# Optimization experiments

Measured on AMD Instinct MI355X. Metric: run time of the kernel, lower is better.

## Reference

```python
import jax, jax.numpy as jnp
import numpy as np

# Grids: sparse_shape=(41,320,320); after spcv1 stride(2,1,1) pad1 k3 -> (21,320,320);
# after spcv2 stride(2,1,1) pad(0,1,1) k3 -> (10,320,320); after spcv3 k(3,1,1) stride(2,1,1) -> (4,320,320)
GRID0 = (41, 320, 320)
GRID1 = (21, 320, 320)
GRID2 = (10, 320, 320)
GRID3 = (4, 320, 320)
T = 3
C_IN = 16
BN_EPS = 1e-3


def _idx_grid(coords, shape):
    g = -np.ones(shape, np.int32)
    g[coords[:, 0], coords[:, 1], coords[:, 2]] = np.arange(len(coords), dtype=np.int32)
    return g


def _subm_nbrs(coords, grid):
    M = len(coords)
    nbr = -np.ones((M, 27), np.int32)
    sh = np.array(grid.shape)
    k = 0
    for dz in (-1, 0, 1):
        for dy in (-1, 0, 1):
            for dx in (-1, 0, 1):
                c = coords + np.array([dz, dy, dx])
                ok = np.all((c >= 0) & (c < sh), axis=1)
                nbr[ok, k] = grid[c[ok, 0], c[ok, 1], c[ok, 2]]
                k += 1
    return nbr


def _spconv_pairs(coords_in, grid_in, out_shape, ksz, stride, pad):
    ksz = np.array(ksz); st = np.array(stride); pd = np.array(pad); osh = np.array(out_shape)
    cands = []
    for kz in range(ksz[0]):
        for ky in range(ksz[1]):
            for kx in range(ksz[2]):
                o = coords_in + pd - np.array([kz, ky, kx])
                ok = np.all(o % st == 0, axis=1)
                o = o[ok] // st
                ok2 = np.all((o >= 0) & (o < osh), axis=1)
                cands.append(o[ok2])
    coords_out = np.unique(np.concatenate(cands, 0), axis=0)
    M = len(coords_out); K = int(np.prod(ksz))
    idx = -np.ones((M, K), np.int32)
    sh = np.array(grid_in.shape)
    k = 0
    for kz in range(ksz[0]):
        for ky in range(ksz[1]):
            for kx in range(ksz[2]):
                ci = coords_out * st - pd + np.array([kz, ky, kx])
                ok = np.all((ci >= 0) & (ci < sh), axis=1)
                idx[ok, k] = grid_in[ci[ok, 0], ci[ok, 1], ci[ok, 2]]
                k += 1
    return coords_out.astype(np.int32), idx


def setup_inputs() -> dict:
    rng = np.random.default_rng(0)
    # clustered lidar-like active voxels
    nC, nP = 60, 150
    centers = np.stack([rng.uniform(6, 35, nC), rng.uniform(12, 308, nC), rng.uniform(12, 308, nC)], 1)
    pts = centers[:, None, :] + rng.normal(size=(nC, nP, 3)) * np.array([1.2, 2.0, 2.0])
    pts = np.clip(np.round(pts).astype(np.int64).reshape(-1, 3), 0, np.array(GRID0) - 1)
    coords0 = np.unique(pts, axis=0)
    g0 = _idx_grid(coords0, GRID0)
    nbr0 = _subm_nbrs(coords0, g0)
    coords1, idx1 = _spconv_pairs(coords0, g0, GRID1, (3, 3, 3), (2, 1, 1), (1, 1, 1))
    g1 = _idx_grid(coords1, GRID1)
    nbr1 = _subm_nbrs(coords1, g1)
    coords2, idx2 = _spconv_pairs(coords1, g1, GRID2, (3, 3, 3), (2, 1, 1), (0, 1, 1))
    g2 = _idx_grid(coords2, GRID2)
    nbr2 = _subm_nbrs(coords2, g2)
    coords3, idx3 = _spconv_pairs(coords2, g2, GRID3, (3, 1, 1), (2, 1, 1), (0, 0, 0))

    def w(K, ci, co):
        return jnp.asarray(rng.standard_normal((K, ci, co)) / np.sqrt(K * ci), jnp.float32)

    def bn(n, c):
        g = rng.uniform(0.5, 1.5, (n, c)); b = rng.standard_normal((n, c)) * 0.1
        m = rng.standard_normal((n, c)) * 0.1; v = rng.uniform(0.5, 1.5, (n, c))
        return jnp.asarray(np.stack([g, b, m, v], 1), jnp.float32)  # [n,4,c]

    return dict(
        voxel_features=jnp.asarray(rng.standard_normal((T, len(coords0), C_IN)), jnp.float32),
        w_subm1=w(27, 16, 32), w_subm2=w(27, 32, 32), w_spcv1=w(27, 32, 64),
        w_subm3=w(27, 64, 64), w_subm4=w(27, 64, 64), w_subm5=w(27, 64, 64),
        w_spcv2=w(27, 64, 64), w_subm6=w(27, 64, 64), w_subm7=w(27, 64, 64), w_subm8=w(27, 64, 64),
        w_spcv3=w(3, 64, 64),
        w_ad1=jnp.asarray(rng.standard_normal((64, 64)) / 8.0, jnp.float32),
        w_ad2=jnp.asarray(rng.standard_normal((64, 64)) / 8.0, jnp.float32),
        bn32=bn(2, 32), bn64=bn(9, 64), bn_ad=bn(1, 64)[0],
        nbr0=jnp.asarray(nbr0), idx1=jnp.asarray(idx1), nbr1=jnp.asarray(nbr1),
        idx2=jnp.asarray(idx2), nbr2=jnp.asarray(nbr2), idx3=jnp.asarray(idx3),
        coords3=jnp.asarray(coords3))


def _bn_eval(x, p):
    g, b, m, v = p
    return (x - m) * (g * jax.lax.rsqrt(v + BN_EPS)) + b


def _gconv(f, idx, w):
    # gather-GEMM: idx [M,K] (-1 = missing), f [Min,Ci], w [K,Ci,Co]
    g = jnp.where((idx >= 0)[:, :, None], f[jnp.clip(idx, 0)], 0.0)  # [M,K,Ci]
    return jnp.einsum('mki,kio->mo', g, w)


def reference(voxel_features, w_subm1, w_subm2, w_spcv1, w_subm3, w_subm4, w_subm5,
              w_spcv2, w_subm6, w_subm7, w_subm8, w_spcv3, w_ad1, w_ad2,
              bn32, bn64, bn_ad, nbr0, idx1, nbr1, idx2, nbr2, idx3, coords3):
    relu = jax.nn.relu
    s0 = s1 = s2 = None  # cached previous-frame sparse features per level
    outs = []
    for t in range(voxel_features.shape[0]):
        a0 = 0.0 if s0 is None else jnp.mean(s0, 0)
        a1 = 0.0 if s1 is None else jnp.mean(s1, 0)
        a2 = 0.0 if s2 is None else jnp.mean(s2, 0)
        x = relu(_bn_eval(_gconv(voxel_features[t], nbr0, w_subm1), bn32[0]))
        x = relu(_bn_eval(_gconv(x, nbr0, w_subm2), bn32[1]))
        x3 = relu(_bn_eval(_gconv(x, idx1, w_spcv1) + a0, bn64[0])); s0 = x3
        x = relu(_bn_eval(_gconv(x3, nbr1, w_subm3), bn64[1]))
        x = relu(_bn_eval(_gconv(x, nbr1, w_subm4), bn64[2]))
        x6 = relu(_bn_eval(_gconv(x, nbr1, w_subm5), bn64[3]))
        x7 = relu(_bn_eval(_gconv(x6, idx2, w_spcv2) + a1, bn64[4])); s1 = x7
        x = relu(_bn_eval(_gconv(x7, nbr2, w_subm6), bn64[5]))
        x = relu(_bn_eval(_gconv(x, nbr2, w_subm7), bn64[6]))
        x10 = relu(_bn_eval(_gconv(x, nbr2, w_subm8), bn64[7]))
        x11 = relu(_bn_eval(_gconv(x10, idx3, w_spcv3) + a2, bn64[8])); s2 = x11
        dense = jnp.zeros(GRID3 + (64,), x11.dtype).at[coords3[:, 0], coords3[:, 1], coords3[:, 2]].set(x11)
        outs.append(dense.transpose(3, 0, 1, 2).reshape(1, 64 * GRID3[0], GRID3[1], GRID3[2]))
        adapt = lambda s: (relu(_bn_eval(s @ w_ad1, bn_ad)) @ w_ad2) / 10.0
        s0, s1, s2 = adapt(s0), adapt(s1), adapt(s2)
    return jnp.stack(outs)
```

## Files before the change

### kernel.cpp

```cpp
#include <hip/hip_runtime.h>


typedef _Float16 f16;
typedef _Float16 f16x8 __attribute__((ext_vector_type(8)));
typedef _Float16 f16x4 __attribute__((ext_vector_type(4)));
typedef float    f32x4 __attribute__((ext_vector_type(4)));

#define BN_EPS_F 1e-3f

__global__ __launch_bounds__(256)
void fill_zero(float4* __restrict__ p, long n4)
{
    long i  = blockIdx.x * 256L + threadIdx.x;
    long st = gridDim.x * 256L;
    float4 z = make_float4(0.f, 0.f, 0.f, 0.f);
    for (; i < n4; i += st) p[i] = z;
}

__global__ __launch_bounds__(256)
void wxform(const float* __restrict__ w, f16* __restrict__ wT, int K, int Ci, int Co)
{
    int i = blockIdx.x * 256 + threadIdx.x;
    int total = K * Ci * Co;
    if (i >= total) return;
    int k  = i / (Ci * Co);
    int r  = i - k * (Ci * Co);
    int ci = r / Co;
    int co = r - ci * Co;
    wT[((size_t)k * Co + co) * Ci + ci] = (f16)w[i];
}

template<int Ci, int Co, int K>
__global__ __launch_bounds__(512)
void gconv_mfma(const f16* __restrict__ fin, const int* __restrict__ idx,
                const f16* __restrict__ wT,
                const float* __restrict__ bnp,
                const float* __restrict__ avec,
                f16* __restrict__ fout, int M)
{
    constexpr int CiP = Ci + 8;
    constexpr int cpr = Ci / 8;
    constexpr int NF  = Co / 16;
    constexpr int KK  = Ci / 32;
    constexpr int KH  = (K + 1) / 2;

    __shared__ f16 Ab[2][64 * CiP];
    __shared__ f16 Bb[2][Co * CiP];

    const int tid  = threadIdx.x;
    const int lane = tid & 63;
    const int wv   = tid >> 6;
    const int g    = wv >> 2;
    const int wq   = wv & 3;
    const int gtid = tid & 255;
    const int m0   = blockIdx.x * 64;
    const int l15  = lane & 15;
    const int kg   = lane >> 4;

    f32x4 acc[NF];
    #pragma unroll
    for (int nf = 0; nf < NF; ++nf) acc[nf] = (f32x4){0.f, 0.f, 0.f, 0.f};

    for (int it = 0; it < KH; ++it) {
        const int  k   = (g == 0) ? it : (KH + it);
        const bool act = (g == 0) || (k < K);
        __syncthreads();
        if (act) {
            for (int i = gtid; i < 64 * cpr; i += 256) {
                int r = i / cpr, q = i - r * cpr;
                int m = m0 + r;
                int n = (m < M) ? idx[(size_t)m * K + k] : -1;
                uint4 v = make_uint4(0u, 0u, 0u, 0u);
                if (n >= 0) v = *(const uint4*)&fin[(size_t)n * Ci + q * 8];
                *(uint4*)&Ab[g][r * CiP + q * 8] = v;
            }
            for (int i = gtid; i < Co * cpr; i += 256) {
                int co = i / cpr, q = i - co * cpr;
                *(uint4*)&Bb[g][co * CiP + q * 8] =
                    *(const uint4*)&wT[((size_t)k * Co + co) * Ci + q * 8];
            }
        }
        __syncthreads();
        if (act) {
            #pragma unroll
            for (int kk = 0; kk < KK; ++kk) {
                f16x8 af = *(const f16x8*)&Ab[g][(wq * 16 + l15) * CiP + kk * 32 + kg * 8];
                #pragma unroll
                for (int nf = 0; nf < NF; ++nf) {
                    f16x8 bf = *(const f16x8*)&Bb[g][(nf * 16 + l15) * CiP + kk * 32 + kg * 8];
                    acc[nf] = __builtin_amdgcn_mfma_f32_16x16x32_f16(af, bf, acc[nf], 0, 0, 0);
                }
            }
        }
    }

    float* red = (float*)&Ab[0][0];
    __syncthreads();
    if (g == 1) {
        #pragma unroll
        for (int nf = 0; nf < NF; ++nf)
            #pragma unroll
            for (int j = 0; j < 4; ++j)
                red[(wq * 16 + kg * 4 + j) * Co + nf * 16 + l15] = acc[nf][j];
    }
    __syncthreads();
    if (g == 0) {
        #pragma unroll
        for (int nf = 0; nf < NF; ++nf) {
            int c = nf * 16 + l15;
            float gg = bnp[c], bb = bnp[Co + c], mu = bnp[2 * Co + c], vv = bnp[3 * Co + c];
            float sc = gg * rsqrtf(vv + BN_EPS_F);
            float sh = bb - mu * sc;
            float av = avec ? avec[c] : 0.f;
            #pragma unroll
            for (int j = 0; j < 4; ++j) {
                int row = wq * 16 + kg * 4 + j;
                int m = m0 + row;
                if (m < M) {
                    float x = acc[nf][j] + red[row * Co + c] + av;
                    fout[(size_t)m * Co + c] = (f16)fmaxf(fmaf(x, sc, sh), 0.f);
                }
            }
        }
    }
}

__global__ __launch_bounds__(128)
void gconv16_32(const float* __restrict__ fin, const int* __restrict__ idx,
                const float* __restrict__ w, const float* __restrict__ bnp,
                f16* __restrict__ fout, int M)
{
    __shared__ float fT[16][64];
    __shared__ float wsh[16 * 32];
    const int tx  = threadIdx.x;
    const int ty  = threadIdx.y;
    const int tid = ty * 8 + tx;
    const int m0  = blockIdx.x * 64;

    float acc[4][4] = {};

    for (int k = 0; k < 27; ++k) {
        __syncthreads();
        *(float4*)&wsh[tid * 4] = *(const float4*)&w[(size_t)k * 512 + tid * 4];
        for (int i = tid; i < 64 * 4; i += 128) {
            int r = i >> 2, q = i & 3;
            int m = m0 + r;
            int n = (m < M) ? idx[(size_t)m * 27 + k] : -1;
            float4 v = make_float4(0.f, 0.f, 0.f, 0.f);
            if (n >= 0) v = *(const float4*)&fin[(size_t)n * 16 + q * 4];
            fT[q*4+0][r] = v.x; fT[q*4+1][r] = v.y;
            fT[q*4+2][r] = v.z; fT[q*4+3][r] = v.w;
        }
        __syncthreads();
        #pragma unroll
        for (int ci = 0; ci < 16; ++ci) {
            float4 fv = *(const float4*)&fT[ci][4 * ty];
            float4 wv = *(const float4*)&wsh[ci * 32 + 4 * tx];
            float fr[4] = {fv.x, fv.y, fv.z, fv.w};
            float wr[4] = {wv.x, wv.y, wv.z, wv.w};
            #pragma unroll
            for (int a = 0; a < 4; ++a)
                #pragma unroll
                for (int b = 0; b < 4; ++b)
                    acc[a][b] = fmaf(fr[a], wr[b], acc[a][b]);
        }
    }

    float scale[4], shift[4];
    #pragma unroll
    for (int u = 0; u < 4; ++u) {
        int c = 4 * tx + u;
        float gg = bnp[c], bb = bnp[32 + c], mu = bnp[64 + c], vv = bnp[96 + c];
        float s = gg * rsqrtf(vv + BN_EPS_F);
        scale[u] = s;
        shift[u] = bb - mu * s;
    }
    #pragma unroll
    for (int a = 0; a < 4; ++a) {
        int m = m0 + 4 * ty + a;
        if (m < M) {
            f16x4 o;
            #pragma unroll
            for (int u = 0; u < 4; ++u)
                o[u] = (f16)fmaxf(fmaf(acc[a][u], scale[u], shift[u]), 0.f);
            *(f16x4*)&fout[(size_t)m * 32 + 4 * tx] = o;
        }
    }
}

__global__ __launch_bounds__(64)
void adapt_partial(const f16* __restrict__ s, const float* __restrict__ w_ad1,
                   const float* __restrict__ bn_ad, float* __restrict__ hsum, int M)
{
    __shared__ float wl[64 * 64];
    const int c = threadIdx.x;
    for (int i = c; i < 64 * 64; i += 64) wl[i] = w_ad1[i];
    float gg = bn_ad[c], bb = bn_ad[64 + c], mu = bn_ad[128 + c], vv = bn_ad[192 + c];
    float sc = gg * rsqrtf(vv + BN_EPS_F);
    float sh = bb - mu * sc;
    __syncthreads();

    float hacc = 0.f;
    int r0 = blockIdx.x * 64;
    int r1 = min(r0 + 64, M);
    for (int r = r0; r < r1; ++r) {
        float acc = 0.f;
        #pragma unroll
        for (int i8 = 0; i8 < 8; ++i8) {
            f16x8 sv = *(const f16x8*)&s[(size_t)r * 64 + i8 * 8];
            #pragma unroll
            for (int e = 0; e < 8; ++e)
                acc = fmaf((float)sv[e], wl[(i8 * 8 + e) * 64 + c], acc);
        }
        hacc += fmaxf(fmaf(acc, sc, sh), 0.f);
    }
    atomicAdd(&hsum[c], hacc);
}

__global__ __launch_bounds__(64)
void adapt_finalize(const float* __restrict__ hsum, const float* __restrict__ w_ad2,
                    float* __restrict__ a, float invM)
{
    const int c = threadIdx.x;
    float acc = 0.f;
    #pragma unroll 8
    for (int j = 0; j < 64; ++j) acc = fmaf(hsum[j], w_ad2[j * 64 + c], acc);
    a[c] = (acc * invM) * 0.1f;
}

__global__ __launch_bounds__(64)
void scatter_out(const f16* __restrict__ x11, const int* __restrict__ coords,
                 float* __restrict__ out)
{
    const int m = blockIdx.x;
    const int c = threadIdx.x;
    int z = coords[m * 3 + 0], y = coords[m * 3 + 1], x = coords[m * 3 + 2];
    out[(size_t)(c * 4 + z) * (320 * 320) + y * 320 + x] = (float)x11[(size_t)m * 64 + c];
}

extern "C" void kernel_launch(void* const* d_in, const int* in_sizes, int n_in,
                              void* d_out, int out_size, void* d_ws, size_t ws_size,
                              hipStream_t stream)
{
    const float* vf      = (const float*)d_in[0];
    const float* w_subm1 = (const float*)d_in[1];
    const float* w_subm2 = (const float*)d_in[2];
    const float* w_spcv1 = (const float*)d_in[3];
    const float* w_subm3 = (const float*)d_in[4];
    const float* w_subm4 = (const float*)d_in[5];
    const float* w_subm5 = (const float*)d_in[6];
    const float* w_spcv2 = (const float*)d_in[7];
    const float* w_subm6 = (const float*)d_in[8];
    const float* w_subm7 = (const float*)d_in[9];
    const float* w_subm8 = (const float*)d_in[10];
    const float* w_spcv3 = (const float*)d_in[11];
    const float* w_ad1   = (const float*)d_in[12];
    const float* w_ad2   = (const float*)d_in[13];
    const float* bn32    = (const float*)d_in[14];
    const float* bn64    = (const float*)d_in[15];
    const float* bn_ad   = (const float*)d_in[16];
    const int* nbr0    = (const int*)d_in[17];
    const int* idx1    = (const int*)d_in[18];
    const int* nbr1    = (const int*)d_in[19];
    const int* idx2    = (const int*)d_in[20];
    const int* nbr2    = (const int*)d_in[21];
    const int* idx3    = (const int*)d_in[22];
    const int* coords3 = (const int*)d_in[23];

    const int M0 = in_sizes[0]  / (3 * 16);
    const int M1 = in_sizes[18] / 27;
    const int M2 = in_sizes[20] / 27;
    const int M3 = in_sizes[22] / 3;

    char* base = (char*)d_ws;
    size_t off = 0;
    auto alloc = [&](size_t bytes) -> void* {
        void* p = base + off;
        off = (off + bytes + 255) & ~(size_t)255;
        return p;
    };
    f16* wt_subm2 = (f16*)alloc((size_t)27 * 32 * 32 * 2);
    f16* wt_spcv1 = (f16*)alloc((size_t)27 * 32 * 64 * 2);
    f16* wt_subm3 = (f16*)alloc((size_t)27 * 64 * 64 * 2);
    f16* wt_subm4 = (f16*)alloc((size_t)27 * 64 * 64 * 2);
    f16* wt_subm5 = (f16*)alloc((size_t)27 * 64 * 64 * 2);
    f16* wt_spcv2 = (f16*)alloc((size_t)27 * 64 * 64 * 2);
    f16* wt_subm6 = (f16*)alloc((size_t)27 * 64 * 64 * 2);
    f16* wt_subm7 = (f16*)alloc((size_t)27 * 64 * 64 * 2);
    f16* wt_subm8 = (f16*)alloc((size_t)27 * 64 * 64 * 2);
    f16* wt_spcv3 = (f16*)alloc((size_t)3  * 64 * 64 * 2);
    f16* buf0a = (f16*)alloc((size_t)M0 * 32 * 2);
    f16* buf0b = (f16*)alloc((size_t)M0 * 32 * 2);
    f16* x3    = (f16*)alloc((size_t)M1 * 64 * 2);
    f16* buf1a = (f16*)alloc((size_t)M1 * 64 * 2);
    f16* buf1b = (f16*)alloc((size_t)M1 * 64 * 2);
    f16* x7    = (f16*)alloc((size_t)M2 * 64 * 2);
    f16* buf2a = (f16*)alloc((size_t)M2 * 64 * 2);
    f16* buf2b = (f16*)alloc((size_t)M2 * 64 * 2);
    f16* x11   = (f16*)alloc((size_t)M3 * 64 * 2);
    float* av  = (float*)alloc(192 * 4);
    float* hs  = (float*)alloc(192 * 4);
    (void)ws_size; (void)n_in;

    auto wx = [&](const float* w, f16* wt, int K, int Ci, int Co) {
        int total = K * Ci * Co;
        wxform<<<(total + 255) / 256, 256, 0, stream>>>(w, wt, K, Ci, Co);
    };
    wx(w_subm2, wt_subm2, 27, 32, 32);
    wx(w_spcv1, wt_spcv1, 27, 32, 64);
    wx(w_subm3, wt_subm3, 27, 64, 64);
    wx(w_subm4, wt_subm4, 27, 64, 64);
    wx(w_subm5, wt_subm5, 27, 64, 64);
    wx(w_spcv2, wt_spcv2, 27, 64, 64);
    wx(w_subm6, wt_subm6, 27, 64, 64);
    wx(w_subm7, wt_subm7, 27, 64, 64);
    wx(w_subm8, wt_subm8, 27, 64, 64);
    wx(w_spcv3, wt_spcv3, 3, 64, 64);

    fill_zero<<<2048, 256, 0, stream>>>((float4*)d_out, (long)out_size / 4);

    const int g0 = (M0 + 63) / 64;
    const int g1 = (M1 + 63) / 64;
    const int g2 = (M2 + 63) / 64;
    const int g3 = (M3 + 63) / 64;

    for (int t = 0; t < 3; ++t) {
        const float* vft = vf + (size_t)t * M0 * 16;
        const float* a0 = (t == 0) ? nullptr : av + 0;
        const float* a1 = (t == 0) ? nullptr : av + 64;
        const float* a2 = (t == 0) ? nullptr : av + 128;

        gconv16_32<<<g0, dim3(8, 16), 0, stream>>>(vft, nbr0, w_subm1, bn32, buf0a, M0);
        gconv_mfma<32,32,27><<<g0, 512, 0, stream>>>(buf0a, nbr0, wt_subm2, bn32 + 128,  nullptr, buf0b, M0);
        gconv_mfma<32,64,27><<<g1, 512, 0, stream>>>(buf0b, idx1, wt_spcv1, bn64 + 0,    a0,      x3,    M1);
        gconv_mfma<64,64,27><<<g1, 512, 0, stream>>>(x3,    nbr1, wt_subm3, bn64 + 256,  nullptr, buf1a, M1);
        gconv_mfma<64,64,27><<<g1, 512, 0, stream>>>(buf1a, nbr1, wt_subm4, bn64 + 512,  nullptr, buf1b, M1);
        gconv_mfma<64,64,27><<<g1, 512, 0, stream>>>(buf1b, nbr1, wt_subm5, bn64 + 768,  nullptr, buf1a, M1);
        gconv_mfma<64,64,27><<<g2, 512, 0, stream>>>(buf1a, idx2, wt_spcv2, bn64 + 1024, a1,      x7,    M2);
        gconv_mfma<64,64,27><<<g2, 512, 0, stream>>>(x7,    nbr2, wt_subm6, bn64 + 1280, nullptr, buf2a, M2);
        gconv_mfma<64,64,27><<<g2, 512, 0, stream>>>(buf2a, nbr2, wt_subm7, bn64 + 1536, nullptr, buf2b, M2);
        gconv_mfma<64,64,27><<<g2, 512, 0, stream>>>(buf2b, nbr2, wt_subm8, bn64 + 1792, nullptr, buf2a, M2);
        gconv_mfma<64,64,3><<<g3,  512, 0, stream>>>(buf2a, idx3, wt_spcv3, bn64 + 2048, a2,      x11,   M3);

        scatter_out<<<M3, 64, 0, stream>>>(x11, coords3,
                                           (float*)d_out + (size_t)t * 256 * 320 * 320);

        if (t < 2) {
            hipMemsetAsync(hs, 0, 192 * sizeof(float), stream);
            adapt_partial<<<g1, 64, 0, stream>>>(x3,  w_ad1, bn_ad, hs + 0,   M1);
            adapt_partial<<<g2, 64, 0, stream>>>(x7,  w_ad1, bn_ad, hs + 64,  M2);
            adapt_partial<<<g3, 64, 0, stream>>>(x11, w_ad1, bn_ad, hs + 128, M3);
            adapt_finalize<<<1, 64, 0, stream>>>(hs + 0,   w_ad2, av + 0,   1.f / M1);
            adapt_finalize<<<1, 64, 0, stream>>>(hs + 64,  w_ad2, av + 64,  1.f / M2);
            adapt_finalize<<<1, 64, 0, stream>>>(hs + 128, w_ad2, av + 128, 1.f / M3);
        }
    }
}
```

Baseline: 1.363 ms.

## Rewrite sparse conv pipeline with direct-gather MFMA, batched frames, fused scatter

Replaces the LDS-staged gather conv with a kernel that caches neighbor indices in shared memory and loads A and B fragments directly from global memory. K offsets are split across 4 wave groups with an LDS reduction, and rows per block drop to 32. The frame-independent first two layers run once for all three frames, with the first layer moved onto MFMA via padded f16 input. Weight transforms are merged into one launch, the scatter is fused into the last conv, and the adapter kernels are merged with deterministic partial sums. The risk is more global and L2 traffic for weight fragments and gathered features, since they are no longer reused through LDS.

```diff
diff --git a/kernel.cpp b/kernel.cpp
--- a/kernel.cpp
+++ b/kernel.cpp
@@ -3,7 +3,6 @@
 
 typedef _Float16 f16;
 typedef _Float16 f16x8 __attribute__((ext_vector_type(8)));
-typedef _Float16 f16x4 __attribute__((ext_vector_type(4)));
 typedef float    f32x4 __attribute__((ext_vector_type(4)));
 
 #define BN_EPS_F 1e-3f
@@ -12,98 +11,130 @@
 void fill_zero(float4* __restrict__ p, long n4)
 {
     long i  = blockIdx.x * 256L + threadIdx.x;
-    long st = gridDim.x * 256L;
+    long st = (long)gridDim.x * 256L;
     float4 z = make_float4(0.f, 0.f, 0.f, 0.f);
     for (; i < n4; i += st) p[i] = z;
 }
 
 __global__ __launch_bounds__(256)
-void wxform(const float* __restrict__ w, f16* __restrict__ wT, int K, int Ci, int Co)
+void vf_convert(const float* __restrict__ vf, f16* __restrict__ vf16, int nrows)
 {
     int i = blockIdx.x * 256 + threadIdx.x;
-    int total = K * Ci * Co;
+    if (i >= nrows * 32) return;
+    int r = i >> 5, c = i & 31;
+    vf16[i] = (c < 16) ? (f16)vf[r * 16 + c] : (f16)0;
+}
+
+struct WXA { const float* s; f16* d; int K, Ci, Co, CiD, off; };
+struct WXAll { WXA w[11]; };
+
+__global__ __launch_bounds__(256)
+void wxform_all(WXAll wa, int total)
+{
+    int i = blockIdx.x * 256 + threadIdx.x;
     if (i >= total) return;
-    int k  = i / (Ci * Co);
-    int r  = i - k * (Ci * Co);
-    int ci = r / Co;
-    int co = r - ci * Co;
-    wT[((size_t)k * Co + co) * Ci + ci] = (f16)w[i];
-}
-
-template<int Ci, int Co, int K>
-__global__ __launch_bounds__(512)
-void gconv_mfma(const f16* __restrict__ fin, const int* __restrict__ idx,
-                const f16* __restrict__ wT,
-                const float* __restrict__ bnp,
-                const float* __restrict__ avec,
-                f16* __restrict__ fout, int M)
-{
-    constexpr int CiP = Ci + 8;
-    constexpr int cpr = Ci / 8;
+    int j = 0;
+    #pragma unroll
+    for (int t = 1; t < 11; ++t) if (i >= wa.w[t].off) j = t;
+    const float* s = wa.w[j].s;
+    f16* d = wa.w[j].d;
+    int Ci = wa.w[j].Ci, Co = wa.w[j].Co, CiD = wa.w[j].CiD;
+    int e = i - wa.w[j].off;
+    int cc = Co * CiD;
+    int k = e / cc; int rem = e - k * cc;
+    int co = rem / CiD; int ci = rem - co * CiD;
+    float v = (ci < Ci) ? s[((size_t)k * Ci + ci) * Co + co] : 0.f;
+    d[e] = (f16)v;
+}
+
+template<int Ci, int Co, int K, int ROWS, int KSPLIT, bool SCATTER>
+__global__ __launch_bounds__((ROWS/16)*KSPLIT*64)
+void gconv(const f16* __restrict__ fin, const int* __restrict__ idx,
+           const f16* __restrict__ wT,
+           const float* __restrict__ bnp,
+           const float* __restrict__ avec,
+           f16* __restrict__ fout,
+           const int* __restrict__ coords, float* __restrict__ dout,
+           int M, int blocksPerFrame, long finStride, long foutStride)
+{
+    constexpr int RW  = ROWS / 16;
+    constexpr int NW  = RW * KSPLIT;
+    constexpr int NT  = NW * 64;
     constexpr int NF  = Co / 16;
     constexpr int KK  = Ci / 32;
-    constexpr int KH  = (K + 1) / 2;
-
-    __shared__ f16 Ab[2][64 * CiP];
-    __shared__ f16 Bb[2][Co * CiP];
+    constexpr int TPG = (K + KSPLIT - 1) / KSPLIT;
+    constexpr int CoP = Co + 4;
+
+    __shared__ int   sIdx[ROWS][K];
+    __shared__ float red[KSPLIT > 1 ? KSPLIT - 1 : 1][ROWS][CoP];
 
     const int tid  = threadIdx.x;
     const int lane = tid & 63;
-    const int wv   = tid >> 6;
-    const int g    = wv >> 2;
-    const int wq   = wv & 3;
-    const int gtid = tid & 255;
-    const int m0   = blockIdx.x * 64;
+    const int w    = tid >> 6;
+    const int wq   = w % RW;
+    const int g    = w / RW;
     const int l15  = lane & 15;
     const int kg   = lane >> 4;
+
+    const int bid   = blockIdx.x;
+    const int frame = bid / blocksPerFrame;
+    const int fb    = bid - frame * blocksPerFrame;
+    const f16* finF = fin + (long)frame * finStride;
+    f16* foutF      = fout + (long)frame * foutStride;
+    const int m0    = fb * ROWS;
+
+    for (int i = tid; i < ROWS * K; i += NT) {
+        int r = i / K, k = i - r * K;
+        int m = m0 + r;
+        sIdx[r][k] = (m < M) ? idx[(long)m * K + k] : -1;
+    }
+    __syncthreads();
 
     f32x4 acc[NF];
     #pragma unroll
     for (int nf = 0; nf < NF; ++nf) acc[nf] = (f32x4){0.f, 0.f, 0.f, 0.f};
 
-    for (int it = 0; it < KH; ++it) {
-        const int  k   = (g == 0) ? it : (KH + it);
-        const bool act = (g == 0) || (k < K);
+    const int arow = wq * 16 + l15;
+    const int k0 = g * TPG;
+
+    #pragma unroll
+    for (int kt = 0; kt < TPG; ++kt) {
+        int k = k0 + kt;
+        if (k >= K) break;
+        int n = sIdx[arow][k];
+        #pragma unroll
+        for (int kk = 0; kk < KK; ++kk) {
+            f16x8 af = {};
+            if (n >= 0)
+                af = *(const f16x8*)&finF[(long)n * Ci + kk * 32 + kg * 8];
+            #pragma unroll
+            for (int nf = 0; nf < NF; ++nf) {
+                f16x8 bf = *(const f16x8*)&wT[((long)k * Co + nf * 16 + l15) * Ci + kk * 32 + kg * 8];
+                acc[nf] = __builtin_amdgcn_mfma_f32_16x16x32_f16(af, bf, acc[nf], 0, 0, 0);
+            }
+        }
+    }
+
+    if (KSPLIT > 1) {
+        if (g > 0) {
+            #pragma unroll
+            for (int nf = 0; nf < NF; ++nf)
+                #pragma unroll
+                for (int j = 0; j < 4; ++j)
+                    red[g - 1][wq * 16 + kg * 4 + j][nf * 16 + l15] = acc[nf][j];
+        }
         __syncthreads();
-        if (act) {
-            for (int i = gtid; i < 64 * cpr; i += 256) {
-                int r = i / cpr, q = i - r * cpr;
-                int m = m0 + r;
-                int n = (m < M) ? idx[(size_t)m * K + k] : -1;
-                uint4 v = make_uint4(0u, 0u, 0u, 0u);
-                if (n >= 0) v = *(const uint4*)&fin[(size_t)n * Ci + q * 8];
-                *(uint4*)&Ab[g][r * CiP + q * 8] = v;
-            }
-            for (int i = gtid; i < Co * cpr; i += 256) {
-                int co = i / cpr, q = i - co * cpr;
-                *(uint4*)&Bb[g][co * CiP + q * 8] =
-                    *(const uint4*)&wT[((size_t)k * Co + co) * Ci + q * 8];
-            }
-        }
-        __syncthreads();
-        if (act) {
-            #pragma unroll
-            for (int kk = 0; kk < KK; ++kk) {
-                f16x8 af = *(const f16x8*)&Ab[g][(wq * 16 + l15) * CiP + kk * 32 + kg * 8];
+        if (g == 0) {
+            #pragma unroll
+            for (int nf = 0; nf < NF; ++nf)
                 #pragma unroll
-                for (int nf = 0; nf < NF; ++nf) {
-                    f16x8 bf = *(const f16x8*)&Bb[g][(nf * 16 + l15) * CiP + kk * 32 + kg * 8];
-                    acc[nf] = __builtin_amdgcn_mfma_f32_16x16x32_f16(af, bf, acc[nf], 0, 0, 0);
-                }
-            }
-        }
-    }
-
-    float* red = (float*)&Ab[0][0];
-    __syncthreads();
-    if (g == 1) {
-        #pragma unroll
-        for (int nf = 0; nf < NF; ++nf)
-            #pragma unroll
-            for (int j = 0; j < 4; ++j)
-                red[(wq * 16 + kg * 4 + j) * Co + nf * 16 + l15] = acc[nf][j];
-    }
-    __syncthreads();
+                for (int j = 0; j < 4; ++j)
+                    #pragma unroll
+                    for (int gi = 0; gi < KSPLIT - 1; ++gi)
+                        acc[nf][j] += red[gi][wq * 16 + kg * 4 + j][nf * 16 + l15];
+        }
+    }
+
     if (g == 0) {
         #pragma unroll
         for (int nf = 0; nf < NF; ++nf) {
@@ -117,80 +148,27 @@
                 int row = wq * 16 + kg * 4 + j;
                 int m = m0 + row;
                 if (m < M) {
-                    float x = acc[nf][j] + red[row * Co + c] + av;
-                    fout[(size_t)m * Co + c] = (f16)fmaxf(fmaf(x, sc, sh), 0.f);
+                    float x = acc[nf][j] + av;
+                    float y = fmaxf(fmaf(x, sc, sh), 0.f);
+                    foutF[(long)m * Co + c] = (f16)y;
+                    if (SCATTER) {
+                        int z  = coords[m * 3 + 0];
+                        int yy = coords[m * 3 + 1];
+                        int xx = coords[m * 3 + 2];
+                        dout[(long)(c * 4 + z) * (320 * 320) + yy * 320 + xx] = y;
+                    }
                 }
             }
         }
     }
 }
 
-__global__ __launch_bounds__(128)
-void gconv16_32(const float* __restrict__ fin, const int* __restrict__ idx,
-                const float* __restrict__ w, const float* __restrict__ bnp,
-                f16* __restrict__ fout, int M)
-{
-    __shared__ float fT[16][64];
-    __shared__ float wsh[16 * 32];
-    const int tx  = threadIdx.x;
-    const int ty  = threadIdx.y;
-    const int tid = ty * 8 + tx;
-    const int m0  = blockIdx.x * 64;
-
-    float acc[4][4] = {};
-
-    for (int k = 0; k < 27; ++k) {
-        __syncthreads();
-        *(float4*)&wsh[tid * 4] = *(const float4*)&w[(size_t)k * 512 + tid * 4];
-        for (int i = tid; i < 64 * 4; i += 128) {
-            int r = i >> 2, q = i & 3;
-            int m = m0 + r;
-            int n = (m < M) ? idx[(size_t)m * 27 + k] : -1;
-            float4 v = make_float4(0.f, 0.f, 0.f, 0.f);
-            if (n >= 0) v = *(const float4*)&fin[(size_t)n * 16 + q * 4];
-            fT[q*4+0][r] = v.x; fT[q*4+1][r] = v.y;
-            fT[q*4+2][r] = v.z; fT[q*4+3][r] = v.w;
-        }
-        __syncthreads();
-        #pragma unroll
-        for (int ci = 0; ci < 16; ++ci) {
-            float4 fv = *(const float4*)&fT[ci][4 * ty];
-            float4 wv = *(const float4*)&wsh[ci * 32 + 4 * tx];
-            float fr[4] = {fv.x, fv.y, fv.z, fv.w};
-            float wr[4] = {wv.x, wv.y, wv.z, wv.w};
-            #pragma unroll
-            for (int a = 0; a < 4; ++a)
-                #pragma unroll
-                for (int b = 0; b < 4; ++b)
-                    acc[a][b] = fmaf(fr[a], wr[b], acc[a][b]);
-        }
-    }
-
-    float scale[4], shift[4];
-    #pragma unroll
-    for (int u = 0; u < 4; ++u) {
-        int c = 4 * tx + u;
-        float gg = bnp[c], bb = bnp[32 + c], mu = bnp[64 + c], vv = bnp[96 + c];
-        float s = gg * rsqrtf(vv + BN_EPS_F);
-        scale[u] = s;
-        shift[u] = bb - mu * s;
-    }
-    #pragma unroll
-    for (int a = 0; a < 4; ++a) {
-        int m = m0 + 4 * ty + a;
-        if (m < M) {
-            f16x4 o;
-            #pragma unroll
-            for (int u = 0; u < 4; ++u)
-                o[u] = (f16)fmaxf(fmaf(acc[a][u], scale[u], shift[u]), 0.f);
-            *(f16x4*)&fout[(size_t)m * 32 + 4 * tx] = o;
-        }
-    }
-}
-
 __global__ __launch_bounds__(64)
-void adapt_partial(const f16* __restrict__ s, const float* __restrict__ w_ad1,
-                   const float* __restrict__ bn_ad, float* __restrict__ hsum, int M)
+void adapt_partial3(const f16* __restrict__ x3, const f16* __restrict__ x7,
+                    const f16* __restrict__ x11,
+                    const float* __restrict__ w_ad1, const float* __restrict__ bn_ad,
+                    float* __restrict__ pb,
+                    int M1, int M2, int M3, int g1, int g2)
 {
     __shared__ float wl[64 * 64];
     const int c = threadIdx.x;
@@ -200,8 +178,13 @@
     float sh = bb - mu * sc;
     __syncthreads();
 
+    int b = blockIdx.x;
+    const f16* s; int M, r0;
+    if (b < g1)           { s = x3;  M = M1; r0 = b * 64; }
+    else if (b < g1 + g2) { s = x7;  M = M2; r0 = (b - g1) * 64; }
+    else                  { s = x11; M = M3; r0 = (b - g1 - g2) * 64; }
+
     float hacc = 0.f;
-    int r0 = blockIdx.x * 64;
     int r1 = min(r0 + 64, M);
     for (int r = r0; r < r1; ++r) {
         float acc = 0.f;
@@ -214,28 +197,28 @@
         }
         hacc += fmaxf(fmaf(acc, sc, sh), 0.f);
     }
-    atomicAdd(&hsum[c], hacc);
-}
-
-__global__ __launch_bounds__(64)
-void adapt_finalize(const float* __restrict__ hsum, const float* __restrict__ w_ad2,
-                    float* __restrict__ a, float invM)
-{
-    const int c = threadIdx.x;
+    pb[(size_t)b * 64 + c] = hacc;
+}
+
+__global__ __launch_bounds__(192)
+void adapt_final3(const float* __restrict__ pb, const float* __restrict__ w_ad2,
+                  float* __restrict__ av, int g1, int g2, int g3,
+                  float invM1, float invM2, float invM3)
+{
+    __shared__ float h[3][64];
+    const int lvl = threadIdx.x >> 6;
+    const int c   = threadIdx.x & 63;
+    int base = (lvl == 0) ? 0 : (lvl == 1 ? g1 : g1 + g2);
+    int n    = (lvl == 0) ? g1 : (lvl == 1 ? g2 : g3);
+    float invM = (lvl == 0) ? invM1 : (lvl == 1 ? invM2 : invM3);
     float acc = 0.f;
+    for (int i = 0; i < n; ++i) acc += pb[(size_t)(base + i) * 64 + c];
+    h[lvl][c] = acc * invM;
+    __syncthreads();
+    float o = 0.f;
     #pragma unroll 8
-    for (int j = 0; j < 64; ++j) acc = fmaf(hsum[j], w_ad2[j * 64 + c], acc);
-    a[c] = (acc * invM) * 0.1f;
-}
-
-__global__ __launch_bounds__(64)
-void scatter_out(const f16* __restrict__ x11, const int* __restrict__ coords,
-                 float* __restrict__ out)
-{
-    const int m = blockIdx.x;
-    const int c = threadIdx.x;
-    int z = coords[m * 3 + 0], y = coords[m * 3 + 1], x = coords[m * 3 + 2];
-    out[(size_t)(c * 4 + z) * (320 * 320) + y * 320 + x] = (float)x11[(size_t)m * 64 + c];
+    for (int j = 0; j < 64; ++j) o = fmaf(h[lvl][j], w_ad2[j * 64 + c], o);
+    av[lvl * 64 + c] = o * 0.1f;
 }
 
 extern "C" void kernel_launch(void* const* d_in, const int* in_sizes, int n_in,
@@ -279,18 +262,20 @@
         off = (off + bytes + 255) & ~(size_t)255;
         return p;
     };
-    f16* wt_subm2 = (f16*)alloc((size_t)27 * 32 * 32 * 2);
-    f16* wt_spcv1 = (f16*)alloc((size_t)27 * 32 * 64 * 2);
-    f16* wt_subm3 = (f16*)alloc((size_t)27 * 64 * 64 * 2);
-    f16* wt_subm4 = (f16*)alloc((size_t)27 * 64 * 64 * 2);
-    f16* wt_subm5 = (f16*)alloc((size_t)27 * 64 * 64 * 2);
-    f16* wt_spcv2 = (f16*)alloc((size_t)27 * 64 * 64 * 2);
-    f16* wt_subm6 = (f16*)alloc((size_t)27 * 64 * 64 * 2);
-    f16* wt_subm7 = (f16*)alloc((size_t)27 * 64 * 64 * 2);
-    f16* wt_subm8 = (f16*)alloc((size_t)27 * 64 * 64 * 2);
-    f16* wt_spcv3 = (f16*)alloc((size_t)3  * 64 * 64 * 2);
-    f16* buf0a = (f16*)alloc((size_t)M0 * 32 * 2);
-    f16* buf0b = (f16*)alloc((size_t)M0 * 32 * 2);
+    f16* wt1  = (f16*)alloc((size_t)27 * 32 * 32 * 2);
+    f16* wt2  = (f16*)alloc((size_t)27 * 32 * 32 * 2);
+    f16* wtc1 = (f16*)alloc((size_t)27 * 64 * 32 * 2);
+    f16* wt3  = (f16*)alloc((size_t)27 * 64 * 64 * 2);
+    f16* wt4  = (f16*)alloc((size_t)27 * 64 * 64 * 2);
+    f16* wt5  = (f16*)alloc((size_t)27 * 64 * 64 * 2);
+    f16* wtc2 = (f16*)alloc((size_t)27 * 64 * 64 * 2);
+    f16* wt6  = (f16*)alloc((size_t)27 * 64 * 64 * 2);
+    f16* wt7  = (f16*)alloc((size_t)27 * 64 * 64 * 2);
+    f16* wt8  = (f16*)alloc((size_t)27 * 64 * 64 * 2);
+    f16* wtc3 = (f16*)alloc((size_t)3  * 64 * 64 * 2);
+    f16* vf16  = (f16*)alloc((size_t)3 * M0 * 32 * 2);
+    f16* buf0a = (f16*)alloc((size_t)3 * M0 * 32 * 2);
+    f16* buf0b = (f16*)alloc((size_t)3 * M0 * 32 * 2);
     f16* x3    = (f16*)alloc((size_t)M1 * 64 * 2);
     f16* buf1a = (f16*)alloc((size_t)M1 * 64 * 2);
     f16* buf1b = (f16*)alloc((size_t)M1 * 64 * 2);
@@ -299,60 +284,72 @@
     f16* buf2b = (f16*)alloc((size_t)M2 * 64 * 2);
     f16* x11   = (f16*)alloc((size_t)M3 * 64 * 2);
     float* av  = (float*)alloc(192 * 4);
-    float* hs  = (float*)alloc(192 * 4);
+    const int g1a = (M1 + 63) / 64, g2a = (M2 + 63) / 64, g3a = (M3 + 63) / 64;
+    float* pb  = (float*)alloc((size_t)(g1a + g2a + g3a) * 64 * 4);
     (void)ws_size; (void)n_in;
 
-    auto wx = [&](const float* w, f16* wt, int K, int Ci, int Co) {
-        int total = K * Ci * Co;
-        wxform<<<(total + 255) / 256, 256, 0, stream>>>(w, wt, K, Ci, Co);
+    WXAll wa;
+    int woff = 0;
+    auto addw = [&](int slot, const float* s, f16* d, int K, int Ci, int Co, int CiD) {
+        wa.w[slot] = {s, d, K, Ci, Co, CiD, woff};
+        woff += K * Co * CiD;
     };
-    wx(w_subm2, wt_subm2, 27, 32, 32);
-    wx(w_spcv1, wt_spcv1, 27, 32, 64);
-    wx(w_subm3, wt_subm3, 27, 64, 64);
-    wx(w_subm4, wt_subm4, 27, 64, 64);
-    wx(w_subm5, wt_subm5, 27, 64, 64);
-    wx(w_spcv2, wt_spcv2, 27, 64, 64);
-    wx(w_subm6, wt_subm6, 27, 64, 64);
-    wx(w_subm7, wt_subm7, 27, 64, 64);
-    wx(w_subm8, wt_subm8, 27, 64, 64);
-    wx(w_spcv3, wt_spcv3, 3, 64, 64);
-
+    addw(0,  w_subm1, wt1,  27, 16, 32, 32);
+    addw(1,  w_subm2, wt2,  27, 32, 32, 32);
+    addw(2,  w_spcv1, wtc1, 27, 32, 64, 32);
+    addw(3,  w_subm3, wt3,  27, 64, 64, 64);
+    addw(4,  w_subm4, wt4,  27, 64, 64, 64);
+    addw(5,  w_subm5, wt5,  27, 64, 64, 64);
+    addw(6,  w_spcv2, wtc2, 27, 64, 64, 64);
+    addw(7,  w_subm6, wt6,  27, 64, 64, 64);
+    addw(8,  w_subm7, wt7,  27, 64, 64, 64);
+    addw(9,  w_subm8, wt8,  27, 64, 64, 64);
+    addw(10, w_spcv3, wtc3, 3,  64, 64, 64);
+    wxform_all<<<(woff + 255) / 256, 256, 0, stream>>>(wa, woff);
+    vf_convert<<<(3 * M0 * 32 + 255) / 256, 256, 0, stream>>>(vf, vf16, 3 * M0);
     fill_zero<<<2048, 256, 0, stream>>>((float4*)d_out, (long)out_size / 4);
 
-    const int g0 = (M0 + 63) / 64;
-    const int g1 = (M1 + 63) / 64;
-    const int g2 = (M2 + 63) / 64;
-    const int g3 = (M3 + 63) / 64;
+    const int g0w = (M0 + 31) / 32;
+    const int g1w = (M1 + 31) / 32;
+    const int g2w = (M2 + 31) / 32;
+    const int g3w = (M3 + 31) / 32;
+    const long s0 = (long)M0 * 32;
+
+    gconv<32,32,27,32,4,false><<<3 * g0w, 512, 0, stream>>>(
+        vf16,  nbr0, wt1, bn32,       nullptr, buf0a, nullptr, nullptr, M0, g0w, s0, s0);
+    gconv<32,32,27,32,4,false><<<3 * g0w, 512, 0, stream>>>(
+        buf0a, nbr0, wt2, bn32 + 128, nullptr, buf0b, nullptr, nullptr, M0, g0w, s0, s0);
 
     for (int t = 0; t < 3; ++t) {
-        const float* vft = vf + (size_t)t * M0 * 16;
         const float* a0 = (t == 0) ? nullptr : av + 0;
         const float* a1 = (t == 0) ? nullptr : av + 64;
         const float* a2 = (t == 0) ? nullptr : av + 128;
-
-        gconv16_32<<<g0, dim3(8, 16), 0, stream>>>(vft, nbr0, w_subm1, bn32, buf0a, M0);
-        gconv_mfma<32,32,27><<<g0, 512, 0, stream>>>(buf0a, nbr0, wt_subm2, bn32 + 128,  nullptr, buf0b, M0);
-        gconv_mfma<32,64,27><<<g1, 512, 0, stream>>>(buf0b, idx1, wt_spcv1, bn64 + 0,    a0,      x3,    M1);
-        gconv_mfma<64,64,27><<<g1, 512, 0, stream>>>(x3,    nbr1, wt_subm3, bn64 + 256,  nullptr, buf1a, M1);
-        gconv_mfma<64,64,27><<<g1, 512, 0, stream>>>(buf1a, nbr1, wt_subm4, bn64 + 512,  nullptr, buf1b, M1);
-        gconv_mfma<64,64,27><<<g1, 512, 0, stream>>>(buf1b, nbr1, wt_subm5, bn64 + 768,  nullptr, buf1a, M1);
-        gconv_mfma<64,64,27><<<g2, 512, 0, stream>>>(buf1a, idx2, wt_spcv2, bn64 + 1024, a1,      x7,    M2);
-        gconv_mfma<64,64,27><<<g2, 512, 0, stream>>>(x7,    nbr2, wt_subm6, bn64 + 1280, nullptr, buf2a, M2);
-        gconv_mfma<64,64,27><<<g2, 512, 0, stream>>>(buf2a, nbr2, wt_subm7, bn64 + 1536, nullptr, buf2b, M2);
-        gconv_mfma<64,64,27><<<g2, 512, 0, stream>>>(buf2b, nbr2, wt_subm8, bn64 + 1792, nullptr, buf2a, M2);
-        gconv_mfma<64,64,3><<<g3,  512, 0, stream>>>(buf2a, idx3, wt_spcv3, bn64 + 2048, a2,      x11,   M3);
-
-        scatter_out<<<M3, 64, 0, stream>>>(x11, coords3,
-                                           (float*)d_out + (size_t)t * 256 * 320 * 320);
+        float* doutT = (float*)d_out + (size_t)t * 256 * 320 * 320;
+
+        gconv<32,64,27,32,4,false><<<g1w, 512, 0, stream>>>(
+            buf0b + (long)t * s0, idx1, wtc1, bn64, a0, x3, nullptr, nullptr, M1, g1w, 0, 0);
+        gconv<64,64,27,32,4,false><<<g1w, 512, 0, stream>>>(
+            x3,    nbr1, wt3, bn64 + 256,  nullptr, buf1a, nullptr, nullptr, M1, g1w, 0, 0);
+        gconv<64,64,27,32,4,false><<<g1w, 512, 0, stream>>>(
+            buf1a, nbr1, wt4, bn64 + 512,  nullptr, buf1b, nullptr, nullptr, M1, g1w, 0, 0);
+        gconv<64,64,27,32,4,false><<<g1w, 512, 0, stream>>>(
+            buf1b, nbr1, wt5, bn64 + 768,  nullptr, buf1a, nullptr, nullptr, M1, g1w, 0, 0);
+        gconv<64,64,27,32,4,false><<<g2w, 512, 0, stream>>>(
+            buf1a, idx2, wtc2, bn64 + 1024, a1,     x7,    nullptr, nullptr, M2, g2w, 0, 0);
+        gconv<64,64,27,32,4,false><<<g2w, 512, 0, stream>>>(
+            x7,    nbr2, wt6, bn64 + 1280, nullptr, buf2a, nullptr, nullptr, M2, g2w, 0, 0);
+        gconv<64,64,27,32,4,false><<<g2w, 512, 0, stream>>>(
+            buf2a, nbr2, wt7, bn64 + 1536, nullptr, buf2b, nullptr, nullptr, M2, g2w, 0, 0);
+        gconv<64,64,27,32,4,false><<<g2w, 512, 0, stream>>>(
+            buf2b, nbr2, wt8, bn64 + 1792, nullptr, buf2a, nullptr, nullptr, M2, g2w, 0, 0);
+        gconv<64,64,3,32,3,true><<<g3w, 384, 0, stream>>>(
+            buf2a, idx3, wtc3, bn64 + 2048, a2,    x11,   coords3, doutT,   M3, g3w, 0, 0);
 
         if (t < 2) {
-            hipMemsetAsync(hs, 0, 192 * sizeof(float), stream);
-            adapt_partial<<<g1, 64, 0, stream>>>(x3,  w_ad1, bn_ad, hs + 0,   M1);
-            adapt_partial<<<g2, 64, 0, stream>>>(x7,  w_ad1, bn_ad, hs + 64,  M2);
-            adapt_partial<<<g3, 64, 0, stream>>>(x11, w_ad1, bn_ad, hs + 128, M3);
-            adapt_finalize<<<1, 64, 0, stream>>>(hs + 0,   w_ad2, av + 0,   1.f / M1);
-            adapt_finalize<<<1, 64, 0, stream>>>(hs + 64,  w_ad2, av + 64,  1.f / M2);
-            adapt_finalize<<<1, 64, 0, stream>>>(hs + 128, w_ad2, av + 128, 1.f / M3);
-        }
-    }
-}
+            adapt_partial3<<<g1a + g2a + g3a, 64, 0, stream>>>(
+                x3, x7, x11, w_ad1, bn_ad, pb, M1, M2, M3, g1a, g2a);
+            adapt_final3<<<1, 192, 0, stream>>>(
+                pb, w_ad2, av, g1a, g2a, g3a, 1.f / M1, 1.f / M2, 1.f / M3);
+        }
+    }
+}
```

Result: slower. 1.674 ms (+22.8%).
